# Performance work log

Hardware: AMD Instinct MI355X
Metric: run time of the kernel (lower is better)

Reference implementation:

```python
import jax, jax.numpy as jnp
import numpy as np

HEADS = 8
EMBED = 64
FEAT_A = 256
FEAT_B = 256


def setup_inputs() -> dict:
    key = jax.random.key(0)
    k1, k2, k3, k4, k5 = jax.random.split(key, 5)
    B, N = 2, 2048
    z_a = jax.random.normal(k1, (B, FEAT_A, N), dtype=jnp.float32)
    z_b = jax.random.normal(k2, (B, FEAT_B, N), dtype=jnp.float32)
    # Conv1d(k=1, bias=False) weights, squeezed: [out_ch, in_ch]
    W_a = jax.random.normal(k3, (HEADS * EMBED, FEAT_A), dtype=jnp.float32) * (1.0 / np.sqrt(FEAT_A))
    W_b = jax.random.normal(k4, (HEADS * EMBED, FEAT_B), dtype=jnp.float32) * (1.0 / np.sqrt(FEAT_B))
    W_c = jax.random.normal(k5, (FEAT_A, HEADS * FEAT_B), dtype=jnp.float32) * (1.0 / np.sqrt(HEADS * FEAT_B))
    return {"z_a": z_a, "z_b": z_b, "W_a": W_a, "W_b": W_b, "W_c": W_c}


def reference(z_a, z_b, W_a, W_b, W_c):
    B, Fa, Na = z_a.shape
    Fb = z_b.shape[1]
    H, E = HEADS, EMBED
    norm = 1.0 / np.sqrt(E)
    # 1x1 conv embeddings -> q, k: [B, H, E, N]
    q = jnp.einsum('of,bfn->bon', W_a, z_a).reshape(B, H, E, Na)
    k = jnp.einsum('of,bfn->bon', W_b, z_b).reshape(B, H, E, -1)
    v = z_b  # [B, Fb, K]
    # coeff_pre_softmax[b,h,q,k] = (q^T k) / sqrt(E)
    pre = jnp.einsum('bheq,bhek->bhqk', q, k) * norm
    coeff = jax.nn.softmax(pre, axis=-1)  # softmax over keys (dim=2 in torch bmm form)
    # l1 loss: mean |pre| over (q,k) per head, averaged over heads
    l1 = jnp.mean(jnp.abs(pre), axis=(1, 2, 3))  # [B]
    # feat[b,h,q,f] = coeff @ v^T
    feat = jnp.einsum('bhqk,bfk->bhqf', coeff, v)
    # combine heads: w[h] = W_c[:, h*Fb:(h+1)*Fb].T  -> [H, Fb, Fa]
    w = W_c.reshape(Fa, H, Fb).transpose(1, 2, 0)
    out = jnp.einsum('bhqf,hfo->bqo', feat, w)  # sum over heads
    return out, l1
```

## Files before the change

### kernel.cpp

```cpp
#include <hip/hip_runtime.h>
#include <hip/hip_bf16.h>


#define B_ 2
#define N_ 2048
#define F_ 256
#define H_ 8
#define E_ 64

typedef __attribute__((ext_vector_type(8))) short bf16x8;
typedef __attribute__((ext_vector_type(4))) float f32x4;

__device__ __forceinline__ unsigned short f2b(float x) {
  __hip_bfloat16 h = __float2bfloat16(x);
  return *reinterpret_cast<unsigned short*>(&h);
}

__device__ __forceinline__ unsigned short f2bt(float x) {
  union { float f; unsigned u; } c; c.f = x;
  return (unsigned short)(c.u >> 16);
}

__device__ __forceinline__ f32x4 mfma16(bf16x8 a, bf16x8 b, f32x4 c) {
  return __builtin_amdgcn_mfma_f32_16x16x32_bf16(a, b, c, 0, 0, 0);
}

__device__ __forceinline__ void async_lds16(const unsigned short* g, unsigned short* l) {
  __builtin_amdgcn_global_load_lds(
      (const __attribute__((address_space(1))) unsigned int*)g,
      (__attribute__((address_space(3))) unsigned int*)l, 16, 0, 0);
}

__global__ __launch_bounds__(256) void prep_kernel(
    const float* __restrict__ z_b, unsigned short* __restrict__ vbf,
    const float* __restrict__ W_c, unsigned short* __restrict__ wcb,
    const float* __restrict__ W_a, const float* __restrict__ W_b,
    unsigned short* __restrict__ wab, float* __restrict__ l1acc) {
  int i = blockIdx.x * 256 + threadIdx.x;
  if (i < B_) l1acc[i] = 0.f;
  const int nzb = B_ * F_ * N_ / 4;
  const int nwc = F_ * H_ * F_ / 4;
  const int nw = 512 * F_ / 4;
  const float* src; unsigned short* dst; int j;
  if (i < nzb) { src = z_b; dst = vbf; j = i; }
  else if (i < nzb + nwc) { src = W_c; dst = wcb; j = i - nzb; }
  else if (i < nzb + nwc + nw) { src = W_a; dst = wab; j = i - nzb - nwc; }
  else { j = i - nzb - nwc - nw; if (j >= nw) return; src = W_b; dst = wab + 512 * F_; }
  float4 v = reinterpret_cast<const float4*>(src)[j];
  unsigned long long pk =
      ((unsigned long long)f2b(v.w) << 48) | ((unsigned long long)f2b(v.z) << 32) |
      ((unsigned long long)f2b(v.y) << 16) | (unsigned long long)f2b(v.x);
  reinterpret_cast<unsigned long long*>(dst)[j] = pk;
}

__global__ __launch_bounds__(256) void transp_kernel(
    const float* __restrict__ z_a, const float* __restrict__ z_b,
    unsigned short* __restrict__ zaT, unsigned short* __restrict__ zbT) {
  __shared__ unsigned int t32[64][65];
  const int tid = threadIdx.x;
  const int nt = blockIdx.x, ft = blockIdx.y, wz = blockIdx.z;
  const int b = wz & 1, which = wz >> 1;
  const float* src = (which ? z_b : z_a) + (size_t)b * F_ * N_;
  unsigned short* dst = (which ? zbT : zaT) + (size_t)b * N_ * F_;
  const int col = tid & 63, rb = tid >> 6;
#pragma unroll
  for (int i = 0; i < 16; ++i) {
    int row = rb + i * 4;
    t32[row][col] = f2b(src[(size_t)(ft * 64 + row) * N_ + nt * 64 + col]);
  }
  __syncthreads();
#pragma unroll
  for (int i = 0; i < 16; ++i) {
    int row = rb + i * 4;
    dst[(size_t)(nt * 64 + row) * F_ + ft * 64 + col] = (unsigned short)t32[col][row];
  }
}

__global__ __launch_bounds__(256) void proj_mfma(
    const unsigned short* __restrict__ zaT, const unsigned short* __restrict__ zbT,
    const unsigned short* __restrict__ wab,
    unsigned short* __restrict__ qT, unsigned short* __restrict__ kT) {
  __shared__ __align__(16) unsigned short As[2][64][32];
  __shared__ __align__(16) unsigned short Bs[2][64][32];

  const int tid = threadIdx.x;
  const int wid = tid >> 6, lane = tid & 63;
  const int quad = lane >> 4, l16 = lane & 15;
  const int nt = blockIdx.x, ot = blockIdx.y, wz = blockIdx.z;
  const int b = wz & 1, which = wz >> 1;

  const unsigned short* zsrc = (which ? zbT : zaT) + (size_t)b * N_ * F_;
  const unsigned short* wsrc = wab + (size_t)which * 512 * F_;
  unsigned short* dst = (which ? kT : qT) + (size_t)b * N_ * 512;
  const float scale = which ? 1.f : 0.125f;

  const int srow = wid * 16 + (lane >> 2);
  const int schunk = (lane & 3) ^ ((srow >> 1) & 3);
  const unsigned short* agl = zsrc + (size_t)(nt * 64 + srow) * F_ + schunk * 8;
  const unsigned short* bgl = wsrc + (size_t)(ot * 64 + srow) * F_ + schunk * 8;
  const int roff = (quad ^ ((l16 >> 1) & 3)) * 8;

  f32x4 acc[4];
  const f32x4 zero4 = {0.f, 0.f, 0.f, 0.f};
#pragma unroll
  for (int g = 0; g < 4; ++g) acc[g] = zero4;

  async_lds16(agl, &As[0][wid * 16][0]);
  async_lds16(bgl, &Bs[0][wid * 16][0]);
  __syncthreads();

#pragma unroll
  for (int kt = 0; kt < 8; ++kt) {
    const int cur = kt & 1;
    if (kt + 1 < 8) {
      async_lds16(agl + (kt + 1) * 32, &As[cur ^ 1][wid * 16][0]);
      async_lds16(bgl + (kt + 1) * 32, &Bs[cur ^ 1][wid * 16][0]);
    }
    bf16x8 bf = *reinterpret_cast<const bf16x8*>(&Bs[cur][0][0] + (wid * 16 + l16) * 32 + roff);
#pragma unroll
    for (int g = 0; g < 4; ++g) {
      bf16x8 af = *reinterpret_cast<const bf16x8*>(&As[cur][0][0] + (g * 16 + l16) * 32 + roff);
      acc[g] = mfma16(af, bf, acc[g]);
    }
    __syncthreads();
  }

#pragma unroll
  for (int g = 0; g < 4; ++g)
#pragma unroll
    for (int r = 0; r < 4; ++r)
      dst[(size_t)(nt * 64 + g * 16 + quad * 4 + r) * 512 + ot * 64 + wid * 16 + l16] =
          f2b(acc[g][r] * scale);
}

__global__ __launch_bounds__(256, 3) void attn_mfma(
    const unsigned short* __restrict__ qT, const unsigned short* __restrict__ kT,
    const unsigned short* __restrict__ vbf, unsigned short* __restrict__ feat,
    float* __restrict__ l1acc) {
  __shared__ __align__(16) unsigned short ks[2][32][64];
  __shared__ __align__(16) unsigned short vs[2][256][32];
  __shared__ __align__(16) unsigned short p_blk[2][64][40];
  __shared__ float lsum_sh[64];
  __shared__ float redblk[256];

  const int tid = threadIdx.x;
  const int wid = tid >> 6, lane = tid & 63;
  const int quad = lane >> 4, l16 = lane & 15;
  const int qt = blockIdx.x, h = blockIdx.y, b = blockIdx.z;

  const int kkey = wid * 8 + (lane >> 3);
  const int kchunk = (lane & 7) ^ ((kkey >> 1) & 7);
  const unsigned short* kgl =
      kT + ((size_t)(b * N_ + kkey) * 512) + h * 64 + kchunk * 8;
  const unsigned short* vgl[4];
#pragma unroll
  for (int j = 0; j < 4; ++j) {
    int f = (wid * 4 + j) * 16 + (lane >> 2);
    int c = (lane & 3) ^ ((f >> 1) & 3);
    vgl[j] = vbf + ((size_t)(b * F_ + f) * 2048) + c * 8;
  }

  const unsigned short* qrow =
      qT + (size_t)(b * N_ + qt * 64 + wid * 16 + l16) * 512 + h * 64 + quad * 8;
  bf16x8 qf0 = *reinterpret_cast<const bf16x8*>(qrow);
  bf16x8 qf1 = *reinterpret_cast<const bf16x8*>(qrow + 32);

  const int koff = ((quad ^ (l16 & 7)) * 8);
  const int voff = ((quad ^ ((l16 >> 1) & 3)) * 8);

  f32x4 acc[4][4];
  const f32x4 zero4 = {0.f, 0.f, 0.f, 0.f};
#pragma unroll
  for (int g = 0; g < 4; ++g)
#pragma unroll
    for (int t = 0; t < 4; ++t) acc[g][t] = zero4;
  float lsum[4] = {0.f, 0.f, 0.f, 0.f};
  float suml1 = 0.f;
  bf16x8 vreg[4];

  async_lds16(kgl, &ks[0][wid * 8][0]);
#pragma unroll
  for (int j = 0; j < 4; ++j) async_lds16(vgl[j], &vs[0][(wid * 4 + j) * 16][0]);
  __syncthreads();

#pragma unroll 2
  for (int kt = 0; kt < N_ / 32; ++kt) {
    const int cur = kt & 1;
    if (kt + 1 < N_ / 32) {
      async_lds16(kgl + (size_t)(kt + 1) * 32 * 512, &ks[cur ^ 1][wid * 8][0]);
#pragma unroll
      for (int j = 0; j < 4; ++j)
        async_lds16(vgl[j] + (kt + 1) * 32, &vs[cur ^ 1][(wid * 4 + j) * 16][0]);
    }

    const unsigned short* ksc = &ks[cur][0][0];
    bf16x8 kf00 = *reinterpret_cast<const bf16x8*>(ksc + (2 * l16) * 64 + koff);
    bf16x8 kf01 = *reinterpret_cast<const bf16x8*>(ksc + (2 * l16) * 64 + (koff ^ 32));
    bf16x8 kf10 = *reinterpret_cast<const bf16x8*>(ksc + (2 * l16 + 1) * 64 + koff);
    bf16x8 kf11 = *reinterpret_cast<const bf16x8*>(ksc + (2 * l16 + 1) * 64 + (koff ^ 32));

    f32x4 s0 = mfma16(qf0, kf00, zero4); s0 = mfma16(qf1, kf01, s0);
    f32x4 s1 = mfma16(qf0, kf10, zero4); s1 = mfma16(qf1, kf11, s1);

#pragma unroll
    for (int r = 0; r < 4; ++r) {
      float a0 = s0[r], a1 = s1[r];
      suml1 += fabsf(a0) + fabsf(a1);
      float p0 = __expf(a0), p1 = __expf(a1);
      lsum[r] += p0 + p1;
      unsigned pk = ((unsigned)f2bt(p1) << 16) | f2bt(p0);
      *reinterpret_cast<unsigned*>(&p_blk[cur][wid * 16 + quad * 4 + r][2 * l16]) = pk;
    }

    if (kt > 0) {
#pragma unroll
      for (int g = 0; g < 4; ++g) {
        bf16x8 pf = *reinterpret_cast<const bf16x8*>(&p_blk[cur ^ 1][g * 16 + l16][quad * 8]);
#pragma unroll
        for (int t = 0; t < 4; ++t) acc[g][t] = mfma16(pf, vreg[t], acc[g][t]);
      }
    }

    {
      const unsigned short* vsc = &vs[cur][0][0];
#pragma unroll
      for (int t = 0; t < 4; ++t) {
        int f = wid * 64 + t * 16 + l16;
        vreg[t] = *reinterpret_cast<const bf16x8*>(vsc + f * 32 + voff);
      }
    }
    __syncthreads();
  }

  {
#pragma unroll
    for (int g = 0; g < 4; ++g) {
      bf16x8 pf = *reinterpret_cast<const bf16x8*>(&p_blk[1][g * 16 + l16][quad * 8]);
#pragma unroll
      for (int t = 0; t < 4; ++t) acc[g][t] = mfma16(pf, vreg[t], acc[g][t]);
    }
  }

#pragma unroll
  for (int r = 0; r < 4; ++r) {
    float rs = lsum[r];
    rs += __shfl_xor(rs, 1);
    rs += __shfl_xor(rs, 2);
    rs += __shfl_xor(rs, 4);
    rs += __shfl_xor(rs, 8);
    if (l16 == 0) lsum_sh[wid * 16 + quad * 4 + r] = rs;
  }
  __syncthreads();

#pragma unroll
  for (int g = 0; g < 4; ++g)
#pragma unroll
    for (int r = 0; r < 4; ++r) {
      float invl = 1.f / lsum_sh[g * 16 + quad * 4 + r];
      unsigned short* fr =
          feat + (size_t)(b * N_ + qt * 64 + g * 16 + quad * 4 + r) * 2048 +
          h * 256 + wid * 64 + l16;
#pragma unroll
      for (int t = 0; t < 4; ++t) fr[t * 16] = f2b(acc[g][t][r] * invl);
    }

  redblk[tid] = suml1;
  __syncthreads();
  for (int st = 128; st > 0; st >>= 1) {
    if (tid < st) redblk[tid] += redblk[tid + st];
    __syncthreads();
  }
  if (tid == 0) atomicAdd(&l1acc[b], redblk[0]);
}

__global__ __launch_bounds__(256) void combine_mfma(
    const unsigned short* __restrict__ feat, const unsigned short* __restrict__ wcb,
    const float* __restrict__ l1acc, float* __restrict__ out) {
  __shared__ __align__(16) unsigned short As[2][64][32];
  __shared__ __align__(16) unsigned short Bs[2][32][32];

  const int tid = threadIdx.x;
  const int wid = tid >> 6, lane = tid & 63;
  const int quad = lane >> 4, l16 = lane & 15;
  const int mb = blockIdx.x, ob = blockIdx.y;
  const int ow = wid & 1, mh = wid >> 1;

  const int srow = wid * 16 + (lane >> 2);
  const int schunk = (lane & 3) ^ ((srow >> 1) & 3);
  const unsigned short* agl = feat + (size_t)(mb * 64 + srow) * 2048 + schunk * 8;
  const unsigned short* bgl = wcb + (size_t)(ob * 32 + srow) * 2048 + schunk * 8;

  const int roff = (quad ^ ((l16 >> 1) & 3)) * 8;

  f32x4 acc[2];
  const f32x4 zero4 = {0.f, 0.f, 0.f, 0.f};
#pragma unroll
  for (int g = 0; g < 2; ++g) acc[g] = zero4;

  async_lds16(agl, &As[0][wid * 16][0]);
  if (wid < 2) async_lds16(bgl, &Bs[0][wid * 16][0]);
  __syncthreads();

#pragma unroll 2
  for (int kt = 0; kt < 64; ++kt) {
    const int cur = kt & 1;
    if (kt + 1 < 64) {
      async_lds16(agl + (kt + 1) * 32, &As[cur ^ 1][wid * 16][0]);
      if (wid < 2) async_lds16(bgl + (kt + 1) * 32, &Bs[cur ^ 1][wid * 16][0]);
    }
    bf16x8 bf = *reinterpret_cast<const bf16x8*>(&Bs[cur][0][0] + (ow * 16 + l16) * 32 + roff);
#pragma unroll
    for (int g = 0; g < 2; ++g) {
      bf16x8 af =
          *reinterpret_cast<const bf16x8*>(&As[cur][0][0] + (mh * 32 + g * 16 + l16) * 32 + roff);
      acc[g] = mfma16(af, bf, acc[g]);
    }
    __syncthreads();
  }

#pragma unroll
  for (int g = 0; g < 2; ++g)
#pragma unroll
    for (int r = 0; r < 4; ++r)
      out[(size_t)(mb * 64 + mh * 32 + g * 16 + quad * 4 + r) * 256 +
          ob * 32 + ow * 16 + l16] = acc[g][r];

  if (mb == 0 && ob == 0 && tid < B_)
    out[(size_t)B_ * N_ * F_ + tid] = l1acc[tid] * (1.f / (float)(H_ * N_ * N_));
}

extern "C" void kernel_launch(void* const* d_in, const int* in_sizes, int n_in,
                              void* d_out, int out_size, void* d_ws, size_t ws_size,
                              hipStream_t stream) {
  const float* z_a = (const float*)d_in[0];
  const float* z_b = (const float*)d_in[1];
  const float* W_a = (const float*)d_in[2];
  const float* W_b = (const float*)d_in[3];
  const float* W_c = (const float*)d_in[4];
  float* out = (float*)d_out;

  char* ws = (char*)d_ws;
  unsigned short* qT = (unsigned short*)ws;
  unsigned short* kT = (unsigned short*)(ws + ((size_t)4 << 20));
  unsigned short* vbf = (unsigned short*)(ws + ((size_t)8 << 20));
  unsigned short* wcb = (unsigned short*)(ws + ((size_t)10 << 20));
  unsigned short* feat = (unsigned short*)(ws + ((size_t)11 << 20));
  float* l1acc = (float*)(ws + ((size_t)27 << 20));
  unsigned short* zaT = (unsigned short*)(ws + ((size_t)28 << 20));
  unsigned short* zbT = (unsigned short*)(ws + ((size_t)30 << 20));
  unsigned short* wab = (unsigned short*)(ws + ((size_t)32 << 20));

  const int nprep = B_ * F_ * N_ / 4 + F_ * H_ * F_ / 4 + 2 * (512 * F_ / 4);
  prep_kernel<<<dim3((nprep + 255) / 256), 256, 0, stream>>>(
      z_b, vbf, W_c, wcb, W_a, W_b, wab, l1acc);
  transp_kernel<<<dim3(N_ / 64, F_ / 64, 4), 256, 0, stream>>>(z_a, z_b, zaT, zbT);
  proj_mfma<<<dim3(N_ / 64, 8, 4), 256, 0, stream>>>(zaT, zbT, wab, qT, kT);
  attn_mfma<<<dim3(N_ / 64, H_, B_), 256, 0, stream>>>(qT, kT, vbf, feat, l1acc);
  combine_mfma<<<dim3(B_ * N_ / 64, 8), 256, 0, stream>>>(feat, wcb, l1acc, out);
}
```

Baseline: 167.7 us.

## Stage full-K A tiles in LDS and read B fragments directly from global

In proj_mfma, the whole 64x256 activation tile is loaded into XOR-swizzled LDS once, and the per-k-step double buffering and barriers are removed. Weight fragments are now read straight from global memory into registers. combine_mfma now computes a 64x64 output per block instead of 64x32, halving the grid's y dimension. It stages 256-wide K chunks of feat with double buffering and reads W_c fragments from global, which cuts barrier count and repeated feat loads. The workspace layout is also reshuffled. The cost is more LDS per block and uncoalesced-per-lane global B reads that depend on cache hits.

```diff
diff --git a/kernel.cpp b/kernel.cpp
--- a/kernel.cpp
+++ b/kernel.cpp
@@ -80,8 +80,7 @@
     const unsigned short* __restrict__ zaT, const unsigned short* __restrict__ zbT,
     const unsigned short* __restrict__ wab,
     unsigned short* __restrict__ qT, unsigned short* __restrict__ kT) {
-  __shared__ __align__(16) unsigned short As[2][64][32];
-  __shared__ __align__(16) unsigned short Bs[2][64][32];
+  __shared__ __align__(16) unsigned short As[64][256];
 
   const int tid = threadIdx.x;
   const int wid = tid >> 6, lane = tid & 63;
@@ -94,35 +93,32 @@
   unsigned short* dst = (which ? kT : qT) + (size_t)b * N_ * 512;
   const float scale = which ? 1.f : 0.125f;
 
-  const int srow = wid * 16 + (lane >> 2);
-  const int schunk = (lane & 3) ^ ((srow >> 1) & 3);
-  const unsigned short* agl = zsrc + (size_t)(nt * 64 + srow) * F_ + schunk * 8;
-  const unsigned short* bgl = wsrc + (size_t)(ot * 64 + srow) * F_ + schunk * 8;
-  const int roff = (quad ^ ((l16 >> 1) & 3)) * 8;
+#pragma unroll
+  for (int i = 0; i < 8; ++i) {
+    int row = wid * 16 + 2 * i + (lane >> 5);
+    int cg = (lane & 31) ^ (row & 31);
+    async_lds16(zsrc + (size_t)(nt * 64 + row) * F_ + cg * 8, &As[wid * 16 + 2 * i][0]);
+  }
+
+  const unsigned short* brow = wsrc + (size_t)(ot * 64 + wid * 16 + l16) * F_ + quad * 8;
 
   f32x4 acc[4];
   const f32x4 zero4 = {0.f, 0.f, 0.f, 0.f};
 #pragma unroll
   for (int g = 0; g < 4; ++g) acc[g] = zero4;
 
-  async_lds16(agl, &As[0][wid * 16][0]);
-  async_lds16(bgl, &Bs[0][wid * 16][0]);
   __syncthreads();
 
 #pragma unroll
   for (int kt = 0; kt < 8; ++kt) {
-    const int cur = kt & 1;
-    if (kt + 1 < 8) {
-      async_lds16(agl + (kt + 1) * 32, &As[cur ^ 1][wid * 16][0]);
-      async_lds16(bgl + (kt + 1) * 32, &Bs[cur ^ 1][wid * 16][0]);
-    }
-    bf16x8 bf = *reinterpret_cast<const bf16x8*>(&Bs[cur][0][0] + (wid * 16 + l16) * 32 + roff);
+    bf16x8 bf = *reinterpret_cast<const bf16x8*>(brow + kt * 32);
 #pragma unroll
     for (int g = 0; g < 4; ++g) {
-      bf16x8 af = *reinterpret_cast<const bf16x8*>(&As[cur][0][0] + (g * 16 + l16) * 32 + roff);
+      int row = g * 16 + l16;
+      int p = (kt * 4 + quad) ^ (row & 31);
+      bf16x8 af = *reinterpret_cast<const bf16x8*>(&As[0][0] + row * 256 + p * 8);
       acc[g] = mfma16(af, bf, acc[g]);
     }
-    __syncthreads();
   }
 
 #pragma unroll
@@ -276,54 +272,62 @@
 __global__ __launch_bounds__(256) void combine_mfma(
     const unsigned short* __restrict__ feat, const unsigned short* __restrict__ wcb,
     const float* __restrict__ l1acc, float* __restrict__ out) {
-  __shared__ __align__(16) unsigned short As[2][64][32];
-  __shared__ __align__(16) unsigned short Bs[2][32][32];
+  __shared__ __align__(16) unsigned short As[2][64][256];
 
   const int tid = threadIdx.x;
   const int wid = tid >> 6, lane = tid & 63;
   const int quad = lane >> 4, l16 = lane & 15;
   const int mb = blockIdx.x, ob = blockIdx.y;
-  const int ow = wid & 1, mh = wid >> 1;
-
-  const int srow = wid * 16 + (lane >> 2);
-  const int schunk = (lane & 3) ^ ((srow >> 1) & 3);
-  const unsigned short* agl = feat + (size_t)(mb * 64 + srow) * 2048 + schunk * 8;
-  const unsigned short* bgl = wcb + (size_t)(ob * 32 + srow) * 2048 + schunk * 8;
-
-  const int roff = (quad ^ ((l16 >> 1) & 3)) * 8;
-
-  f32x4 acc[2];
+
+  const int srow_hi = lane >> 5;
+  const int spos = lane & 31;
+
+  const unsigned short* brow = wcb + (size_t)(ob * 64 + wid * 16 + l16) * 2048 + quad * 8;
+
+  f32x4 acc[4];
   const f32x4 zero4 = {0.f, 0.f, 0.f, 0.f};
 #pragma unroll
-  for (int g = 0; g < 2; ++g) acc[g] = zero4;
-
-  async_lds16(agl, &As[0][wid * 16][0]);
-  if (wid < 2) async_lds16(bgl, &Bs[0][wid * 16][0]);
-  __syncthreads();
-
-#pragma unroll 2
-  for (int kt = 0; kt < 64; ++kt) {
-    const int cur = kt & 1;
-    if (kt + 1 < 64) {
-      async_lds16(agl + (kt + 1) * 32, &As[cur ^ 1][wid * 16][0]);
-      if (wid < 2) async_lds16(bgl + (kt + 1) * 32, &Bs[cur ^ 1][wid * 16][0]);
-    }
-    bf16x8 bf = *reinterpret_cast<const bf16x8*>(&Bs[cur][0][0] + (ow * 16 + l16) * 32 + roff);
-#pragma unroll
-    for (int g = 0; g < 2; ++g) {
-      bf16x8 af =
-          *reinterpret_cast<const bf16x8*>(&As[cur][0][0] + (mh * 32 + g * 16 + l16) * 32 + roff);
-      acc[g] = mfma16(af, bf, acc[g]);
+  for (int g = 0; g < 4; ++g) acc[g] = zero4;
+
+#pragma unroll
+  for (int i = 0; i < 8; ++i) {
+    int row = wid * 16 + 2 * i + srow_hi;
+    int cg = spos ^ (row & 31);
+    async_lds16(feat + (size_t)(mb * 64 + row) * 2048 + cg * 8, &As[0][wid * 16 + 2 * i][0]);
+  }
+  __syncthreads();
+
+  for (int ch = 0; ch < 8; ++ch) {
+    const int cur = ch & 1;
+    if (ch + 1 < 8) {
+#pragma unroll
+      for (int i = 0; i < 8; ++i) {
+        int row = wid * 16 + 2 * i + srow_hi;
+        int cg = spos ^ (row & 31);
+        async_lds16(feat + (size_t)(mb * 64 + row) * 2048 + (ch + 1) * 256 + cg * 8,
+                    &As[cur ^ 1][wid * 16 + 2 * i][0]);
+      }
+    }
+#pragma unroll
+    for (int kt = 0; kt < 8; ++kt) {
+      bf16x8 bf = *reinterpret_cast<const bf16x8*>(brow + ch * 256 + kt * 32);
+#pragma unroll
+      for (int g = 0; g < 4; ++g) {
+        int row = g * 16 + l16;
+        int p = (kt * 4 + quad) ^ (row & 31);
+        bf16x8 af = *reinterpret_cast<const bf16x8*>(&As[cur][0][0] + row * 256 + p * 8);
+        acc[g] = mfma16(af, bf, acc[g]);
+      }
     }
     __syncthreads();
   }
 
 #pragma unroll
-  for (int g = 0; g < 2; ++g)
+  for (int g = 0; g < 4; ++g)
 #pragma unroll
     for (int r = 0; r < 4; ++r)
-      out[(size_t)(mb * 64 + mh * 32 + g * 16 + quad * 4 + r) * 256 +
-          ob * 32 + ow * 16 + l16] = acc[g][r];
+      out[(size_t)(mb * 64 + g * 16 + quad * 4 + r) * 256 + ob * 64 + wid * 16 + l16] =
+          acc[g][r];
 
   if (mb == 0 && ob == 0 && tid < B_)
     out[(size_t)B_ * N_ * F_ + tid] = l1acc[tid] * (1.f / (float)(H_ * N_ * N_));
@@ -344,11 +348,11 @@
   unsigned short* kT = (unsigned short*)(ws + ((size_t)4 << 20));
   unsigned short* vbf = (unsigned short*)(ws + ((size_t)8 << 20));
   unsigned short* wcb = (unsigned short*)(ws + ((size_t)10 << 20));
-  unsigned short* feat = (unsigned short*)(ws + ((size_t)11 << 20));
-  float* l1acc = (float*)(ws + ((size_t)27 << 20));
-  unsigned short* zaT = (unsigned short*)(ws + ((size_t)28 << 20));
-  unsigned short* zbT = (unsigned short*)(ws + ((size_t)30 << 20));
-  unsigned short* wab = (unsigned short*)(ws + ((size_t)32 << 20));
+  unsigned short* zaT = (unsigned short*)(ws + ((size_t)11 << 20));
+  unsigned short* zbT = (unsigned short*)(ws + ((size_t)13 << 20));
+  unsigned short* wab = (unsigned short*)(ws + ((size_t)15 << 20));
+  float* l1acc = (float*)(ws + ((size_t)15 << 20) + (768 << 10));
+  unsigned short* feat = (unsigned short*)(ws + ((size_t)16 << 20));
 
   const int nprep = B_ * F_ * N_ / 4 + F_ * H_ * F_ / 4 + 2 * (512 * F_ / 4);
   prep_kernel<<<dim3((nprep + 255) / 256), 256, 0, stream>>>(
@@ -356,5 +360,5 @@
   transp_kernel<<<dim3(N_ / 64, F_ / 64, 4), 256, 0, stream>>>(z_a, z_b, zaT, zbT);
   proj_mfma<<<dim3(N_ / 64, 8, 4), 256, 0, stream>>>(zaT, zbT, wab, qT, kT);
   attn_mfma<<<dim3(N_ / 64, H_, B_), 256, 0, stream>>>(qT, kT, vbf, feat, l1acc);
-  combine_mfma<<<dim3(B_ * N_ / 64, 8), 256, 0, stream>>>(feat, wcb, l1acc, out);
-}
+  combine_mfma<<<dim3(B_ * N_ / 64, 4), 256, 0, stream>>>(feat, wcb, l1acc, out);
+}
```

New measurement: 163.2 us. 2.7% less time.
